# Performance work log

Hardware: AMD Instinct MI355X
Metric: run time of the kernel (lower is better)

The kernel has to match this reference:

```python
import jax, jax.numpy as jnp
import numpy as np

DIM = 1024
HEADS = 16
DIM_HEAD = 64
INNER = HEADS * DIM_HEAD
SCALE = DIM_HEAD ** -0.5


def rotate_half(t):
    # '... (j d) -> ... j d' with j=2: split last dim in half
    x1, x2 = jnp.split(t, 2, axis=-1)
    return jnp.concatenate((-x2, x1), axis=-1)


def rotary_pos(n, d, dtype):
    inv_freq = 1.0 / (10000.0 ** (jnp.arange(0, d, 2, dtype=jnp.float32) / d))
    freqs = jnp.arange(n, dtype=jnp.float32)[:, None] * inv_freq[None, :]  # (n, d/2)
    return jnp.concatenate((freqs, freqs), axis=-1).astype(dtype)  # (n, d)


def apply_rope(pos, t):
    return t * jnp.cos(pos) + rotate_half(t) * jnp.sin(pos)


def setup_inputs() -> dict:
    key = jax.random.key(0)
    ks = jax.random.split(key, 5)
    x = jax.random.normal(ks[0], (2, 2048, DIM), dtype=jnp.float32)
    gamma = jnp.ones((DIM,), dtype=jnp.float32)
    beta = jnp.zeros((DIM,), dtype=jnp.float32)
    Wq = jax.random.normal(ks[1], (DIM, INNER), dtype=jnp.float32) * 0.02
    Wkv = jax.random.normal(ks[2], (DIM, 2 * INNER), dtype=jnp.float32) * 0.02
    Wo = jax.random.normal(ks[3], (INNER, DIM), dtype=jnp.float32) * 0.02
    return {"x": x, "gamma": gamma, "beta": beta, "Wq": Wq, "Wkv": Wkv, "Wo": Wo}


def reference(x, gamma, beta, Wq, Wkv, Wo):
    b, n, _ = x.shape
    # LayerNorm with learned gamma, fixed-zero beta buffer
    mu = jnp.mean(x, axis=-1, keepdims=True)
    var = jnp.var(x, axis=-1, keepdims=True)
    xn = (x - mu) / jnp.sqrt(var + 1e-5) * gamma + beta

    q = xn @ Wq                       # (b, n, inner)
    kv = xn @ Wkv
    k, v = jnp.split(kv, 2, axis=-1)

    def to_heads(t):
        return t.reshape(b, n, HEADS, DIM_HEAD).transpose(0, 2, 1, 3)  # b h n d

    q, k, v = map(to_heads, (q, k, v))

    pos = rotary_pos(n, DIM_HEAD, x.dtype)  # (n, d)
    q = apply_rope(pos, q)
    k = apply_rope(pos, k)

    q = q * SCALE
    sim = jnp.einsum('bhid,bhjd->bhij', q, k)

    neg = -jnp.finfo(sim.dtype).max
    causal_mask = jnp.triu(jnp.ones((n, n), dtype=bool), k=1)
    sim = jnp.where(causal_mask, neg, sim)

    attn = jax.nn.softmax(sim, axis=-1)
    out = jnp.einsum('bhij,bhjd->bhid', attn, v)
    out = out.transpose(0, 2, 1, 3).reshape(b, n, INNER)
    return out @ Wo
```

## Files before the change

### kernel.cpp

```cpp
#include <hip/hip_runtime.h>
#include <stdint.h>

typedef unsigned short u16;
typedef __attribute__((ext_vector_type(8))) short short8;
typedef __attribute__((ext_vector_type(4))) float floatx4;
typedef __attribute__((ext_vector_type(4))) unsigned short u16x4;
typedef __attribute__((ext_vector_type(2))) unsigned int uint2v;

__device__ __forceinline__ float bf2f(u16 v) {
  union { uint32_t u; float f; } x; x.u = ((uint32_t)v) << 16; return x.f;
}
__device__ __forceinline__ u16 f2bf(float f) {
  union { float f; uint32_t u; } x; x.f = f;
  uint32_t r = x.u + 0x7fffu + ((x.u >> 16) & 1u);
  return (u16)(r >> 16);
}
__device__ __forceinline__ uint32_t fu(float f) {
  union { float f; uint32_t u; } x; x.f = f; return x.u;
}

#define GL2LDS(g, l)                                                          \
  __builtin_amdgcn_global_load_lds(                                           \
      (const __attribute__((address_space(1))) void*)(g),                     \
      (__attribute__((address_space(3))) void*)(l), 16, 0, 0)

__global__ __launch_bounds__(256) void prep_k(const float* __restrict__ x,
                                              const float* __restrict__ gamma,
                                              const float* __restrict__ beta,
                                              const float* __restrict__ Wq,
                                              const float* __restrict__ Wkv,
                                              const float* __restrict__ Wo,
                                              u16* __restrict__ xn,
                                              u16* __restrict__ wqkvT,
                                              u16* __restrict__ woT) {
  int bid = blockIdx.x;
  int t = threadIdx.x;
  if (bid < 4096) {
    int row = bid;
    const float* xr = x + (size_t)row * 1024;
    float4 xv = *(const float4*)(xr + t * 4);
    float v0 = xv.x, v1 = xv.y, v2 = xv.z, v3 = xv.w;
    float s = v0 + v1 + v2 + v3;
    float s2 = v0 * v0 + v1 * v1 + v2 * v2 + v3 * v3;
#pragma unroll
    for (int d = 1; d < 64; d <<= 1) {
      s += __shfl_xor(s, d, 64);
      s2 += __shfl_xor(s2, d, 64);
    }
    __shared__ float red[8];
    int lane = t & 63, wv = t >> 6;
    if (lane == 0) { red[wv] = s; red[4 + wv] = s2; }
    __syncthreads();
    s = red[0] + red[1] + red[2] + red[3];
    s2 = red[4] + red[5] + red[6] + red[7];
    float mu = s * (1.0f / 1024.0f);
    float var = s2 * (1.0f / 1024.0f) - mu * mu;
    float rstd = rsqrtf(var + 1e-5f);
    float4 gv = *(const float4*)(gamma + t * 4);
    float4 bv = *(const float4*)(beta + t * 4);
    u16x4 ov;
    ov.x = f2bf((v0 - mu) * rstd * gv.x + bv.x);
    ov.y = f2bf((v1 - mu) * rstd * gv.y + bv.y);
    ov.z = f2bf((v2 - mu) * rstd * gv.z + bv.z);
    ov.w = f2bf((v3 - mu) * rstd * gv.w + bv.w);
    *(u16x4*)(xn + (size_t)row * 1024 + t * 4) = ov;
  } else {
    __shared__ float tile[32][33];
    int wb = bid - 4096;
    const float* in;
    u16* outp;
    int C;
    if (wb < 1024) { in = Wq; outp = wqkvT; C = 1024; }
    else if (wb < 3072) { wb -= 1024; in = Wkv; outp = wqkvT + 1024 * 1024; C = 2048; }
    else { wb -= 3072; in = Wo; outp = woT; C = 1024; }
    int nbx = C >> 5;
    int c0 = (wb % nbx) * 32, r0 = (wb / nbx) * 32;
    int tx = t & 31, ty = t >> 5;
#pragma unroll
    for (int i = 0; i < 32; i += 8)
      tile[ty + i][tx] = in[(size_t)(r0 + ty + i) * C + c0 + tx];
    __syncthreads();
#pragma unroll
    for (int i = 0; i < 32; i += 8)
      outp[(size_t)(c0 + ty + i) * 1024 + r0 + tx] = f2bf(tile[tx][ty + i]);
  }
}

__global__ __launch_bounds__(256) void gemm_qkv_k(const u16* __restrict__ A,
                                                  const u16* __restrict__ BT,
                                                  u16* __restrict__ C) {
  const int K = 1024, lda = 1024, ldc = 3072;
  __shared__ __align__(16) u16 lA[128 * 32];
  __shared__ __align__(16) u16 lB[128 * 32];
  int tid = threadIdx.x;
  int bm = blockIdx.y * 128;
  int bn = blockIdx.x * 128;
  int w = tid >> 6, l = tid & 63;
  int wm = (w >> 1) * 64, wn = (w & 1) * 64;
  int lr = l & 15, lq = l >> 4;
  floatx4 acc[4][4] = {};
  int sr = w * 16 + (l >> 2);
  int sc = (l & 3) * 8;
  for (int k0 = 0; k0 < K; k0 += 32) {
    GL2LDS(A + (size_t)(bm + sr) * lda + k0 + sc, &lA[sr * 32 + sc]);
    GL2LDS(A + (size_t)(bm + sr + 64) * lda + k0 + sc, &lA[(sr + 64) * 32 + sc]);
    GL2LDS(BT + (size_t)(bn + sr) * K + k0 + sc, &lB[sr * 32 + sc]);
    GL2LDS(BT + (size_t)(bn + sr + 64) * K + k0 + sc, &lB[(sr + 64) * 32 + sc]);
    __syncthreads();
    short8 afr[4], bfr[4];
#pragma unroll
    for (int i = 0; i < 4; i++)
      afr[i] = *(const short8*)(&lA[(wm + i * 16 + lr) * 32 + lq * 8]);
#pragma unroll
    for (int i = 0; i < 4; i++)
      bfr[i] = *(const short8*)(&lB[(wn + i * 16 + lr) * 32 + lq * 8]);
#pragma unroll
    for (int mi = 0; mi < 4; mi++)
#pragma unroll
      for (int ni = 0; ni < 4; ni++)
        acc[mi][ni] = __builtin_amdgcn_mfma_f32_16x16x32_bf16(
            afr[mi], bfr[ni], acc[mi][ni], 0, 0, 0);
    __syncthreads();
  }
  int sec = bn >> 10;
  if (sec == 2) {
#pragma unroll
    for (int mi = 0; mi < 4; mi++)
#pragma unroll
      for (int ni = 0; ni < 4; ni++) {
        int col = bn + wn + ni * 16 + lr;
        int cv = col - 2048;
        int row = bm + wm + mi * 16 + lq * 4;
        int bq = row >> 11;
        int n = row & 2047;
        int bh = (bq << 4) | (cv >> 6);
        int d = cv & 63;
        size_t L = ((size_t)(bh * 64 + d) << 11) + n;
        u16x4 ov;
        ov.x = f2bf(acc[mi][ni][0]);
        ov.y = f2bf(acc[mi][ni][1]);
        ov.z = f2bf(acc[mi][ni][2]);
        ov.w = f2bf(acc[mi][ni][3]);
        *(u16x4*)(C + (L >> 10) * 3072 + 2048 + (L & 1023)) = ov;
      }
  } else {
    float QS = (sec == 0) ? 0.125f * 1.44269504088896f : 1.0f;
#pragma unroll
    for (int ni = 0; ni < 2; ni++) {
      int i = ni * 16 + lr;
      float invf = exp2f(-(float)i * 0.4152410118609203f);
#pragma unroll
      for (int mi = 0; mi < 4; mi++)
#pragma unroll
        for (int r = 0; r < 4; r++) {
          int row = bm + wm + mi * 16 + lq * 4 + r;
          int n = row & 2047;
          float ang = (float)n * invf;
          float s_, c_;
          __sincosf(ang, &s_, &c_);
          float x1 = acc[mi][ni][r], x2 = acc[mi][ni + 2][r];
          int col = bn + wn + ni * 16 + lr;
          C[(size_t)row * ldc + col] = f2bf((x1 * c_ - x2 * s_) * QS);
          C[(size_t)row * ldc + col + 32] = f2bf((x2 * c_ + x1 * s_) * QS);
        }
    }
  }
}

__global__ __launch_bounds__(256) void gemm64_bf16_k(const u16* __restrict__ A,
                                                     const u16* __restrict__ BT,
                                                     float* __restrict__ C,
                                                     int K, int lda, int ldc) {
  __shared__ __align__(16) u16 lA[64 * 32];
  __shared__ __align__(16) u16 lB[128 * 32];
  int tid = threadIdx.x;
  int bm = blockIdx.y * 64;
  int bn = blockIdx.x * 128;
  int w = tid >> 6, l = tid & 63;
  int wm = (w >> 1) * 32, wn = (w & 1) * 64;
  int lr = l & 15, lq = l >> 4;
  floatx4 acc[2][4] = {};
  int sr = w * 16 + (l >> 2);
  int sc = (l & 3) * 8;
  for (int k0 = 0; k0 < K; k0 += 32) {
    GL2LDS(A + (size_t)(bm + sr) * lda + k0 + sc, &lA[sr * 32 + sc]);
    GL2LDS(BT + (size_t)(bn + sr) * K + k0 + sc, &lB[sr * 32 + sc]);
    GL2LDS(BT + (size_t)(bn + sr + 64) * K + k0 + sc, &lB[(sr + 64) * 32 + sc]);
    __syncthreads();
    short8 afr[2], bfr[4];
#pragma unroll
    for (int i = 0; i < 2; i++)
      afr[i] = *(const short8*)(&lA[(wm + i * 16 + lr) * 32 + lq * 8]);
#pragma unroll
    for (int i = 0; i < 4; i++)
      bfr[i] = *(const short8*)(&lB[(wn + i * 16 + lr) * 32 + lq * 8]);
#pragma unroll
    for (int mi = 0; mi < 2; mi++)
#pragma unroll
      for (int ni = 0; ni < 4; ni++)
        acc[mi][ni] = __builtin_amdgcn_mfma_f32_16x16x32_bf16(
            afr[mi], bfr[ni], acc[mi][ni], 0, 0, 0);
    __syncthreads();
  }
#pragma unroll
  for (int mi = 0; mi < 2; mi++)
#pragma unroll
    for (int ni = 0; ni < 4; ni++)
#pragma unroll
      for (int r = 0; r < 4; r++) {
        int row = bm + wm + mi * 16 + lq * 4 + r;
        int col = bn + wn + ni * 16 + lr;
        C[(size_t)row * ldc + col] = acc[mi][ni][r];
      }
}

#define LPT 64
#define FIXM 4.0f
__device__ __forceinline__ void attn_tile2(const u16* lK, const u16* lV, u16* lp,
                                           const short8* aq, floatx4* o,
                                           float& l_i, int lr, int lq,
                                           bool diag, int q0, int k0g,
                                           short8 ones) {
  floatx4 s[4];
#pragma unroll
  for (int ni = 0; ni < 4; ni++) {
    floatx4 a = {};
#pragma unroll
    for (int kc = 0; kc < 2; kc++) {
      int R = ni * 16 + lr;
      int c8 = (kc * 4 + lq) ^ (R & 7);
      short8 kf = *(const short8*)&lK[R * 64 + c8 * 8];
      a = __builtin_amdgcn_mfma_f32_16x16x32_bf16(kf, aq[kc], a, 0, 0, 0);
    }
    s[ni] = a;
  }
  if (diag) {
    int qg = q0 + lr;
#pragma unroll
    for (int ni = 0; ni < 4; ni++)
#pragma unroll
      for (int r = 0; r < 4; r++) {
        int kg = k0g + ni * 16 + lq * 4 + r;
        if (kg > qg) s[ni][r] = -1e30f;
      }
  }
  int swz = (lr & 7) << 3;
#pragma unroll
  for (int ni = 0; ni < 4; ni++) {
    float p0 = exp2f(s[ni][0] - FIXM), p1 = exp2f(s[ni][1] - FIXM);
    float p2 = exp2f(s[ni][2] - FIXM), p3 = exp2f(s[ni][3] - FIXM);
    uint2v dw;
    dw.x = __builtin_amdgcn_perm(fu(p1), fu(p0), 0x07060302u);
    dw.y = __builtin_amdgcn_perm(fu(p3), fu(p2), 0x07060302u);
    *(uint2v*)&lp[lr * LPT + ((ni * 16 + lq * 4) ^ swz)] = dw;
  }
  short8 pb0 = *(const short8*)&lp[lr * LPT + ((lq * 8) ^ swz)];
  short8 pb1 = *(const short8*)&lp[lr * LPT + ((32 + lq * 8) ^ swz)];
  floatx4 z = {};
  z = __builtin_amdgcn_mfma_f32_16x16x32_bf16(ones, pb0, z, 0, 0, 0);
  z = __builtin_amdgcn_mfma_f32_16x16x32_bf16(ones, pb1, z, 0, 0, 0);
  l_i += z[0];
#pragma unroll
  for (int di = 0; di < 4; di++) {
    int R = di * 16 + lr;
    int c80 = lq ^ (R & 7);
    int c81 = (4 + lq) ^ (R & 7);
    short8 v0 = *(const short8*)&lV[R * 64 + c80 * 8];
    o[di] = __builtin_amdgcn_mfma_f32_16x16x32_bf16(v0, pb0, o[di], 0, 0, 0);
    short8 v1 = *(const short8*)&lV[R * 64 + c81 * 8];
    o[di] = __builtin_amdgcn_mfma_f32_16x16x32_bf16(v1, pb1, o[di], 0, 0, 0);
  }
}

__global__ __launch_bounds__(256) void attn_k(const u16* __restrict__ qkv,
                                              u16* __restrict__ out) {
  __shared__ __align__(16) u16 lK[2][64 * 64];
  __shared__ __align__(16) u16 lV[2][64 * 64];
  __shared__ __align__(16) u16 lP[4][16 * LPT];
  int bh = blockIdx.x;
  int b = bh >> 4, h = bh & 15;
  int j = blockIdx.y;
  int tid = threadIdx.x;
  int w = tid >> 6, l = tid & 63;
  int lr = l & 15, lq = l >> 4;
  int q0 = j * 64 + w * 16;
  const u16* qb = qkv + (size_t)b * 2048 * 3072 + h * 64;
  const u16* kb = qkv + (size_t)b * 2048 * 3072 + 1024 + h * 64;
  int bh64 = bh * 64;
  short8 aq[2];
  aq[0] = *(const short8*)(qb + (size_t)(q0 + lr) * 3072 + lq * 8);
  aq[1] = *(const short8*)(qb + (size_t)(q0 + lr) * 3072 + 32 + lq * 8);
  short8 ones;
#pragma unroll
  for (int i = 0; i < 8; i++) ones[i] = (short)0x3F80;
  floatx4 o[4] = {};
  float l_ = 0.0f;
  int srow8 = l >> 3;
  int sc8 = (l & 7) ^ srow8;
  u16* lp = &lP[w][0];
  auto stage = [&](int bufi, int kt) {
#pragma unroll
    for (int c = 0; c < 2; c++) {
      int m = w + c * 4;
      int row = m * 8 + srow8;
      GL2LDS(kb + (size_t)(kt * 64 + row) * 3072 + sc8 * 8, &lK[bufi][m * 512]);
      int nn = kt * 64 + sc8 * 8;
      GL2LDS(qkv + (size_t)((bh64 + row) * 2 + (nn >> 10)) * 3072 + 2048 +
                 (nn & 1023),
             &lV[bufi][m * 512]);
    }
  };
  stage(0, 0);
  for (int kt = 0; kt <= j; ++kt) {
    int cur = kt & 1;
    __syncthreads();
    if (kt < j) stage(cur ^ 1, kt + 1);
    attn_tile2(lK[cur], lV[cur], lp, aq, o, l_, lr, lq, kt == j, q0, kt * 64,
               ones);
  }
  float rl = 1.0f / l_;
#pragma unroll
  for (int di = 0; di < 4; di++) {
    uint2v dw;
    u16 a0 = f2bf(o[di][0] * rl), a1 = f2bf(o[di][1] * rl);
    u16 a2 = f2bf(o[di][2] * rl), a3 = f2bf(o[di][3] * rl);
    dw.x = (uint32_t)a0 | ((uint32_t)a1 << 16);
    dw.y = (uint32_t)a2 | ((uint32_t)a3 << 16);
    int dcol = h * 64 + di * 16 + lq * 4;
    *(uint2v*)(out + ((size_t)(b * 2048 + q0 + lr)) * 1024 + dcol) = dw;
  }
}

extern "C" void kernel_launch(void* const* d_in, const int* in_sizes, int n_in,
                              void* d_out, int out_size, void* d_ws, size_t ws_size,
                              hipStream_t stream) {
  const float* x = (const float*)d_in[0];
  const float* gamma = (const float*)d_in[1];
  const float* beta = (const float*)d_in[2];
  const float* Wq = (const float*)d_in[3];
  const float* Wkv = (const float*)d_in[4];
  const float* Wo = (const float*)d_in[5];
  float* out = (float*)d_out;
  char* ws = (char*)d_ws;

  u16* qkv = (u16*)(ws);
  u16* wqkvT = (u16*)(ws + 25165824);
  u16* woT = (u16*)(ws + 31457280);
  u16* xn = (u16*)(ws + 33554432);
  u16* attn_out = xn;

  prep_k<<<8192, 256, 0, stream>>>(x, gamma, beta, Wq, Wkv, Wo, xn, wqkvT, woT);
  gemm_qkv_k<<<dim3(24, 32), 256, 0, stream>>>(xn, wqkvT, qkv);
  attn_k<<<dim3(32, 32), 256, 0, stream>>>(qkv, attn_out);
  gemm64_bf16_k<<<dim3(8, 64), 256, 0, stream>>>(attn_out, woT, out, 1024, 1024, 1024);
}
```

Baseline: 202.6 us.

## Double-buffer LDS staging in GEMMs and reorder causal attention query tiles

Both bf16 GEMM kernels get two LDS buffers. The next K-slice is issued via global_load_lds before computing on the current one, which overlaps global loads with MFMA work and removes one barrier per iteration. The attention kernel remaps blockIdx.y so that odd groups of eight query tiles run in reverse order, spreading the uneven causal workload more evenly across dispatch. The cost is doubled LDS use in the GEMMs, which may lower occupancy.

```diff
diff --git a/kernel.cpp b/kernel.cpp
--- a/kernel.cpp
+++ b/kernel.cpp
@@ -90,8 +90,8 @@
                                                   const u16* __restrict__ BT,
                                                   u16* __restrict__ C) {
   const int K = 1024, lda = 1024, ldc = 3072;
-  __shared__ __align__(16) u16 lA[128 * 32];
-  __shared__ __align__(16) u16 lB[128 * 32];
+  __shared__ __align__(16) u16 lA[2][128 * 32];
+  __shared__ __align__(16) u16 lB[2][128 * 32];
   int tid = threadIdx.x;
   int bm = blockIdx.y * 128;
   int bn = blockIdx.x * 128;
@@ -101,26 +101,31 @@
   floatx4 acc[4][4] = {};
   int sr = w * 16 + (l >> 2);
   int sc = (l & 3) * 8;
-  for (int k0 = 0; k0 < K; k0 += 32) {
-    GL2LDS(A + (size_t)(bm + sr) * lda + k0 + sc, &lA[sr * 32 + sc]);
-    GL2LDS(A + (size_t)(bm + sr + 64) * lda + k0 + sc, &lA[(sr + 64) * 32 + sc]);
-    GL2LDS(BT + (size_t)(bn + sr) * K + k0 + sc, &lB[sr * 32 + sc]);
-    GL2LDS(BT + (size_t)(bn + sr + 64) * K + k0 + sc, &lB[(sr + 64) * 32 + sc]);
-    __syncthreads();
+  auto stage = [&](int bi, int k0) {
+    GL2LDS(A + (size_t)(bm + sr) * lda + k0 + sc, &lA[bi][sr * 32 + sc]);
+    GL2LDS(A + (size_t)(bm + sr + 64) * lda + k0 + sc, &lA[bi][(sr + 64) * 32 + sc]);
+    GL2LDS(BT + (size_t)(bn + sr) * K + k0 + sc, &lB[bi][sr * 32 + sc]);
+    GL2LDS(BT + (size_t)(bn + sr + 64) * K + k0 + sc, &lB[bi][(sr + 64) * 32 + sc]);
+  };
+  stage(0, 0);
+  __syncthreads();
+  for (int it = 0; it < 32; ++it) {
+    int cur = it & 1;
+    if (it < 31) stage(cur ^ 1, (it + 1) * 32);
     short8 afr[4], bfr[4];
 #pragma unroll
     for (int i = 0; i < 4; i++)
-      afr[i] = *(const short8*)(&lA[(wm + i * 16 + lr) * 32 + lq * 8]);
+      afr[i] = *(const short8*)(&lA[cur][(wm + i * 16 + lr) * 32 + lq * 8]);
 #pragma unroll
     for (int i = 0; i < 4; i++)
-      bfr[i] = *(const short8*)(&lB[(wn + i * 16 + lr) * 32 + lq * 8]);
+      bfr[i] = *(const short8*)(&lB[cur][(wn + i * 16 + lr) * 32 + lq * 8]);
 #pragma unroll
     for (int mi = 0; mi < 4; mi++)
 #pragma unroll
       for (int ni = 0; ni < 4; ni++)
         acc[mi][ni] = __builtin_amdgcn_mfma_f32_16x16x32_bf16(
             afr[mi], bfr[ni], acc[mi][ni], 0, 0, 0);
-    __syncthreads();
+    if (it < 31) __syncthreads();
   }
   int sec = bn >> 10;
   if (sec == 2) {
@@ -171,8 +176,8 @@
                                                      const u16* __restrict__ BT,
                                                      float* __restrict__ C,
                                                      int K, int lda, int ldc) {
-  __shared__ __align__(16) u16 lA[64 * 32];
-  __shared__ __align__(16) u16 lB[128 * 32];
+  __shared__ __align__(16) u16 lA[2][64 * 32];
+  __shared__ __align__(16) u16 lB[2][128 * 32];
   int tid = threadIdx.x;
   int bm = blockIdx.y * 64;
   int bn = blockIdx.x * 128;
@@ -182,25 +187,31 @@
   floatx4 acc[2][4] = {};
   int sr = w * 16 + (l >> 2);
   int sc = (l & 3) * 8;
-  for (int k0 = 0; k0 < K; k0 += 32) {
-    GL2LDS(A + (size_t)(bm + sr) * lda + k0 + sc, &lA[sr * 32 + sc]);
-    GL2LDS(BT + (size_t)(bn + sr) * K + k0 + sc, &lB[sr * 32 + sc]);
-    GL2LDS(BT + (size_t)(bn + sr + 64) * K + k0 + sc, &lB[(sr + 64) * 32 + sc]);
-    __syncthreads();
+  auto stage = [&](int bi, int k0) {
+    GL2LDS(A + (size_t)(bm + sr) * lda + k0 + sc, &lA[bi][sr * 32 + sc]);
+    GL2LDS(BT + (size_t)(bn + sr) * K + k0 + sc, &lB[bi][sr * 32 + sc]);
+    GL2LDS(BT + (size_t)(bn + sr + 64) * K + k0 + sc, &lB[bi][(sr + 64) * 32 + sc]);
+  };
+  stage(0, 0);
+  __syncthreads();
+  int NT = K >> 5;
+  for (int it = 0; it < NT; ++it) {
+    int cur = it & 1;
+    if (it + 1 < NT) stage(cur ^ 1, (it + 1) * 32);
     short8 afr[2], bfr[4];
 #pragma unroll
     for (int i = 0; i < 2; i++)
-      afr[i] = *(const short8*)(&lA[(wm + i * 16 + lr) * 32 + lq * 8]);
+      afr[i] = *(const short8*)(&lA[cur][(wm + i * 16 + lr) * 32 + lq * 8]);
 #pragma unroll
     for (int i = 0; i < 4; i++)
-      bfr[i] = *(const short8*)(&lB[(wn + i * 16 + lr) * 32 + lq * 8]);
+      bfr[i] = *(const short8*)(&lB[cur][(wn + i * 16 + lr) * 32 + lq * 8]);
 #pragma unroll
     for (int mi = 0; mi < 2; mi++)
 #pragma unroll
       for (int ni = 0; ni < 4; ni++)
         acc[mi][ni] = __builtin_amdgcn_mfma_f32_16x16x32_bf16(
             afr[mi], bfr[ni], acc[mi][ni], 0, 0, 0);
-    __syncthreads();
+    if (it + 1 < NT) __syncthreads();
   }
 #pragma unroll
   for (int mi = 0; mi < 2; mi++)
@@ -279,7 +290,9 @@
   __shared__ __align__(16) u16 lP[4][16 * LPT];
   int bh = blockIdx.x;
   int b = bh >> 4, h = bh & 15;
-  int j = blockIdx.y;
+  int y = blockIdx.y;
+  int g = y >> 3, o_ = y & 7;
+  int j = (g & 1) ? ((g << 3) + 7 - o_) : y;
   int tid = threadIdx.x;
   int w = tid >> 6, l = tid & 63;
   int lr = l & 15, lq = l >> 4;
```

Result: no change. 204.3 us (+0.8%).

## Double-buffer LDS in GEMM kernels, add MFMA priority hints, reorder attention blocks

Applied to the files above, without the earlier changes.

Both the QKV and output-projection GEMMs now keep two LDS buffers and prefetch the next K-slice with global_load_lds while computing on the current one. The goal is to hide global-load latency behind MFMA work. The attention tile wraps its MFMA sections in s_setprio to favour matrix issue. Attention query-block indices are also remapped so every other group of 8 blocks runs in reverse, which is meant to balance causal work across co-resident blocks. The cost is twice the LDS use in the GEMMs, which may lower occupancy.

```diff
diff --git a/kernel.cpp b/kernel.cpp
--- a/kernel.cpp
+++ b/kernel.cpp
@@ -90,8 +90,8 @@
                                                   const u16* __restrict__ BT,
                                                   u16* __restrict__ C) {
   const int K = 1024, lda = 1024, ldc = 3072;
-  __shared__ __align__(16) u16 lA[128 * 32];
-  __shared__ __align__(16) u16 lB[128 * 32];
+  __shared__ __align__(16) u16 lA[2][128 * 32];
+  __shared__ __align__(16) u16 lB[2][128 * 32];
   int tid = threadIdx.x;
   int bm = blockIdx.y * 128;
   int bn = blockIdx.x * 128;
@@ -101,27 +101,51 @@
   floatx4 acc[4][4] = {};
   int sr = w * 16 + (l >> 2);
   int sc = (l & 3) * 8;
-  for (int k0 = 0; k0 < K; k0 += 32) {
-    GL2LDS(A + (size_t)(bm + sr) * lda + k0 + sc, &lA[sr * 32 + sc]);
-    GL2LDS(A + (size_t)(bm + sr + 64) * lda + k0 + sc, &lA[(sr + 64) * 32 + sc]);
-    GL2LDS(BT + (size_t)(bn + sr) * K + k0 + sc, &lB[sr * 32 + sc]);
-    GL2LDS(BT + (size_t)(bn + sr + 64) * K + k0 + sc, &lB[(sr + 64) * 32 + sc]);
-    __syncthreads();
-    short8 afr[4], bfr[4];
-#pragma unroll
-    for (int i = 0; i < 4; i++)
-      afr[i] = *(const short8*)(&lA[(wm + i * 16 + lr) * 32 + lq * 8]);
-#pragma unroll
-    for (int i = 0; i < 4; i++)
-      bfr[i] = *(const short8*)(&lB[(wn + i * 16 + lr) * 32 + lq * 8]);
-#pragma unroll
-    for (int mi = 0; mi < 4; mi++)
-#pragma unroll
-      for (int ni = 0; ni < 4; ni++)
-        acc[mi][ni] = __builtin_amdgcn_mfma_f32_16x16x32_bf16(
-            afr[mi], bfr[ni], acc[mi][ni], 0, 0, 0);
-    __syncthreads();
-  }
+  int sds = sr * 32 + sc;
+  const u16* pA0 = A + (size_t)(bm + sr) * lda + sc;
+  const u16* pA1 = pA0 + (size_t)64 * lda;
+  const u16* pB0 = BT + (size_t)(bn + sr) * K + sc;
+  const u16* pB1 = pB0 + (size_t)64 * K;
+  int ao[4], bo[4];
+#pragma unroll
+  for (int i = 0; i < 4; i++) {
+    ao[i] = (wm + i * 16 + lr) * 32 + lq * 8;
+    bo[i] = (wn + i * 16 + lr) * 32 + lq * 8;
+  }
+
+#define STAGE_QKV(bi)                                                         \
+  {                                                                           \
+    GL2LDS(pA0, &lA[bi][sds]);                                                \
+    GL2LDS(pA1, &lA[bi][sds + 2048]);                                         \
+    GL2LDS(pB0, &lB[bi][sds]);                                                \
+    GL2LDS(pB1, &lB[bi][sds + 2048]);                                         \
+    pA0 += 32; pA1 += 32; pB0 += 32; pB1 += 32;                               \
+  }
+#define COMPUTE_QKV(bi)                                                       \
+  {                                                                           \
+    short8 afr[4], bfr[4];                                                    \
+    _Pragma("unroll") for (int i = 0; i < 4; i++)                             \
+        afr[i] = *(const short8*)(&lA[bi][ao[i]]);                            \
+    _Pragma("unroll") for (int i = 0; i < 4; i++)                             \
+        bfr[i] = *(const short8*)(&lB[bi][bo[i]]);                            \
+    _Pragma("unroll") for (int mi = 0; mi < 4; mi++)                          \
+        _Pragma("unroll") for (int ni = 0; ni < 4; ni++)                      \
+            acc[mi][ni] = __builtin_amdgcn_mfma_f32_16x16x32_bf16(            \
+                afr[mi], bfr[ni], acc[mi][ni], 0, 0, 0);                      \
+  }
+
+  STAGE_QKV(0);
+  __syncthreads();
+#pragma unroll 1
+  for (int t = 0; t < 16; ++t) {
+    STAGE_QKV(1);
+    COMPUTE_QKV(0);
+    __syncthreads();
+    if (t < 15) STAGE_QKV(0);
+    COMPUTE_QKV(1);
+    __syncthreads();
+  }
+
   int sec = bn >> 10;
   if (sec == 2) {
 #pragma unroll
@@ -171,8 +195,8 @@
                                                      const u16* __restrict__ BT,
                                                      float* __restrict__ C,
                                                      int K, int lda, int ldc) {
-  __shared__ __align__(16) u16 lA[64 * 32];
-  __shared__ __align__(16) u16 lB[128 * 32];
+  __shared__ __align__(16) u16 lA[2][64 * 32];
+  __shared__ __align__(16) u16 lB[2][128 * 32];
   int tid = threadIdx.x;
   int bm = blockIdx.y * 64;
   int bn = blockIdx.x * 128;
@@ -182,24 +206,46 @@
   floatx4 acc[2][4] = {};
   int sr = w * 16 + (l >> 2);
   int sc = (l & 3) * 8;
-  for (int k0 = 0; k0 < K; k0 += 32) {
-    GL2LDS(A + (size_t)(bm + sr) * lda + k0 + sc, &lA[sr * 32 + sc]);
-    GL2LDS(BT + (size_t)(bn + sr) * K + k0 + sc, &lB[sr * 32 + sc]);
-    GL2LDS(BT + (size_t)(bn + sr + 64) * K + k0 + sc, &lB[(sr + 64) * 32 + sc]);
-    __syncthreads();
-    short8 afr[2], bfr[4];
-#pragma unroll
-    for (int i = 0; i < 2; i++)
-      afr[i] = *(const short8*)(&lA[(wm + i * 16 + lr) * 32 + lq * 8]);
-#pragma unroll
-    for (int i = 0; i < 4; i++)
-      bfr[i] = *(const short8*)(&lB[(wn + i * 16 + lr) * 32 + lq * 8]);
-#pragma unroll
-    for (int mi = 0; mi < 2; mi++)
-#pragma unroll
-      for (int ni = 0; ni < 4; ni++)
-        acc[mi][ni] = __builtin_amdgcn_mfma_f32_16x16x32_bf16(
-            afr[mi], bfr[ni], acc[mi][ni], 0, 0, 0);
+  int sds = sr * 32 + sc;
+  const u16* pA0 = A + (size_t)(bm + sr) * lda + sc;
+  const u16* pB0 = BT + (size_t)(bn + sr) * K + sc;
+  const u16* pB1 = pB0 + (size_t)64 * K;
+  int ao[2], bo[4];
+#pragma unroll
+  for (int i = 0; i < 2; i++) ao[i] = (wm + i * 16 + lr) * 32 + lq * 8;
+#pragma unroll
+  for (int i = 0; i < 4; i++) bo[i] = (wn + i * 16 + lr) * 32 + lq * 8;
+
+#define STAGE_O(bi)                                                           \
+  {                                                                           \
+    GL2LDS(pA0, &lA[bi][sds]);                                                \
+    GL2LDS(pB0, &lB[bi][sds]);                                                \
+    GL2LDS(pB1, &lB[bi][sds + 2048]);                                         \
+    pA0 += 32; pB0 += 32; pB1 += 32;                                          \
+  }
+#define COMPUTE_O(bi)                                                         \
+  {                                                                           \
+    short8 afr[2], bfr[4];                                                    \
+    _Pragma("unroll") for (int i = 0; i < 2; i++)                             \
+        afr[i] = *(const short8*)(&lA[bi][ao[i]]);                            \
+    _Pragma("unroll") for (int i = 0; i < 4; i++)                             \
+        bfr[i] = *(const short8*)(&lB[bi][bo[i]]);                            \
+    _Pragma("unroll") for (int mi = 0; mi < 2; mi++)                          \
+        _Pragma("unroll") for (int ni = 0; ni < 4; ni++)                      \
+            acc[mi][ni] = __builtin_amdgcn_mfma_f32_16x16x32_bf16(            \
+                afr[mi], bfr[ni], acc[mi][ni], 0, 0, 0);                      \
+  }
+
+  int NT2 = K >> 6;
+  STAGE_O(0);
+  __syncthreads();
+#pragma unroll 1
+  for (int t = 0; t < NT2; ++t) {
+    STAGE_O(1);
+    COMPUTE_O(0);
+    __syncthreads();
+    if (t < NT2 - 1) STAGE_O(0);
+    COMPUTE_O(1);
     __syncthreads();
   }
 #pragma unroll
@@ -222,6 +268,7 @@
                                            bool diag, int q0, int k0g,
                                            short8 ones) {
   floatx4 s[4];
+  __builtin_amdgcn_s_setprio(1);
 #pragma unroll
   for (int ni = 0; ni < 4; ni++) {
     floatx4 a = {};
@@ -234,6 +281,7 @@
     }
     s[ni] = a;
   }
+  __builtin_amdgcn_s_setprio(0);
   if (diag) {
     int qg = q0 + lr;
 #pragma unroll
@@ -256,6 +304,7 @@
   }
   short8 pb0 = *(const short8*)&lp[lr * LPT + ((lq * 8) ^ swz)];
   short8 pb1 = *(const short8*)&lp[lr * LPT + ((32 + lq * 8) ^ swz)];
+  __builtin_amdgcn_s_setprio(1);
   floatx4 z = {};
   z = __builtin_amdgcn_mfma_f32_16x16x32_bf16(ones, pb0, z, 0, 0, 0);
   z = __builtin_amdgcn_mfma_f32_16x16x32_bf16(ones, pb1, z, 0, 0, 0);
@@ -270,6 +319,7 @@
     short8 v1 = *(const short8*)&lV[R * 64 + c81 * 8];
     o[di] = __builtin_amdgcn_mfma_f32_16x16x32_bf16(v1, pb1, o[di], 0, 0, 0);
   }
+  __builtin_amdgcn_s_setprio(0);
 }
 
 __global__ __launch_bounds__(256) void attn_k(const u16* __restrict__ qkv,
@@ -279,7 +329,9 @@
   __shared__ __align__(16) u16 lP[4][16 * LPT];
   int bh = blockIdx.x;
   int b = bh >> 4, h = bh & 15;
-  int j = blockIdx.y;
+  int y = blockIdx.y;
+  int g = y >> 3, o_ = y & 7;
+  int j = (g & 1) ? ((g << 3) + 7 - o_) : y;
   int tid = threadIdx.x;
   int w = tid >> 6, l = tid & 63;
   int lr = l & 15, lq = l >> 4;
```

Result: no change. 204.1 us (+0.7%).
